# Performance work log

Hardware: AMD Instinct MI355X
Metric: run time of the kernel (lower is better)

## Reference

```python
import jax, jax.numpy as jnp
import numpy as np

B, S, H, E, K = 8, 4096, 1024, 256, 64
NEG = -1e30  # finite stand-in for -inf to keep grads NaN-free


def setup_inputs() -> dict:
    key = jax.random.key(0)
    ks = jax.random.split(key, 8)
    Hq = H // 4
    sc = 0.02
    return {
        "hidden_states": jax.random.normal(ks[0], (B, S, H), dtype=jnp.float32),
        "attention_mask": jnp.ones((B, S), dtype=jnp.int32),
        "block_boundaries": jnp.sort(jax.random.randint(ks[1], (B, K), 0, S), axis=-1),
        "tok_w1": jax.random.normal(ks[2], (H, Hq), dtype=jnp.float32) * sc,
        "tok_b1": jnp.zeros((Hq,), dtype=jnp.float32),
        "tok_w2": jax.random.normal(ks[3], (Hq, 1), dtype=jnp.float32) * sc,
        "tok_b2": jnp.zeros((1,), dtype=jnp.float32),
        "blk_w1": jax.random.normal(ks[4], (H, Hq), dtype=jnp.float32) * sc,
        "blk_b1": jnp.zeros((Hq,), dtype=jnp.float32),
        "blk_w2": jax.random.normal(ks[5], (Hq, 1), dtype=jnp.float32) * sc,
        "blk_b2": jnp.zeros((1,), dtype=jnp.float32),
        "out_w": jax.random.normal(ks[6], (H, E), dtype=jnp.float32) * sc,
        "out_b": jnp.zeros((E,), dtype=jnp.float32),
    }


def _attn_scores(x, w1, b1, w2, b2):
    # Linear -> Tanh -> Linear(.,1), squeeze last dim
    return (jnp.tanh(x @ w1 + b1) @ w2 + b2)[..., 0]


def reference(hidden_states, attention_mask, block_boundaries,
              tok_w1, tok_b1, tok_w2, tok_b2,
              blk_w1, blk_b1, blk_w2, blk_b2,
              out_w, out_b):
    Bz, Sz, Hz = hidden_states.shape
    Kz = block_boundaries.shape[1]
    pos = jnp.arange(Sz)
    # token -> block id: last boundary <= pos (tokens before first boundary get -1)
    block_id = jax.vmap(lambda bnd: jnp.searchsorted(bnd, pos, side='right') - 1)(block_boundaries)  # [B,S]
    member = block_id[:, :, None] == jnp.arange(Kz)[None, None, :]      # [B,S,K]
    valid = (attention_mask == 1) & (block_id >= 0)                     # [B,S]
    m_full = member & valid[:, :, None]                                 # [B,S,K]

    # stage 1: per-block masked softmax over tokens
    tok_scores = _attn_scores(hidden_states, tok_w1, tok_b1, tok_w2, tok_b2)  # [B,S]
    s = jnp.where(m_full, tok_scores[:, :, None], NEG)
    mx = jnp.max(s, axis=1, keepdims=True)                              # [B,1,K]
    e = jnp.where(m_full, jnp.exp(tok_scores[:, :, None] - mx), 0.0)
    denom = jnp.sum(e, axis=1, keepdims=True)                           # [B,1,K]
    w = jnp.where(denom > 0, e / jnp.maximum(denom, 1e-30), 0.0)
    block_embed = jnp.einsum('bsk,bsd->bkd', w, hidden_states)          # [B,K,H]
    block_valid = denom[:, 0, :] > 0                                    # [B,K] (empty blocks dropped)

    # stage 2: softmax over (non-empty) blocks
    blk_scores = _attn_scores(block_embed, blk_w1, blk_b1, blk_w2, blk_b2)    # [B,K]
    blk_scores = jnp.where(block_valid, blk_scores, NEG)
    bw = jax.nn.softmax(blk_scores, axis=-1)
    func = jnp.einsum('bk,bkd->bd', bw, block_embed)                    # [B,H]

    out = func @ out_w + out_b                                          # [B,E]
    return out / jnp.maximum(jnp.linalg.norm(out, axis=-1, keepdims=True), 1e-12)
```

## Files before the change

kernel.cpp:

```cpp
#include <hip/hip_runtime.h>
#include <math.h>
#include <limits.h>

#define BB 8
#define SS 4096
#define HH 1024
#define EE 256
#define KK 64
#define HQ 256
#define NEGF -1e30f

typedef short bf16x8 __attribute__((ext_vector_type(8)));
typedef float f32x4  __attribute__((ext_vector_type(4)));

__device__ inline short f2bf(float x) {
    unsigned u = __float_as_uint(x);
    unsigned r = (u + 0x7fffu + ((u >> 16) & 1u)) >> 16;
    return (short)r;
}

__device__ inline unsigned pk2bf(float lo, float hi) {
    unsigned a = __float_as_uint(lo) + 0x8000u;
    unsigned b = __float_as_uint(hi) + 0x8000u;
    return (a >> 16) | (b & 0xffff0000u);
}

__global__ __launch_bounds__(256) void convert_both_kernel(
    const float* __restrict__ tok_w1, const float* __restrict__ blk_w1,
    short* __restrict__ w1s_tok, short* __restrict__ w1s_blk)
{
    const int kb = blockIdx.x & 31, which = blockIdx.x >> 5;
    const float* src = which ? blk_w1 : tok_w1;
    short* dst = which ? w1s_blk : w1s_tok;
    const int n = threadIdx.x;
    for (int kk = 0; kk < 32; kk++)
        dst[kb * 8192 + n * 32 + kk] = f2bf(src[(kb * 32 + kk) * HQ + n]);
}

__global__ __launch_bounds__(256, 4) void mfma_score4_kernel(
    const float* __restrict__ X, const short* __restrict__ w1s,
    const float* __restrict__ b1, const float* __restrict__ w2,
    const float* __restrict__ b2, float* __restrict__ out)
{
    __shared__ __attribute__((aligned(16))) short As[2][4][1024];
    __shared__ float part[4][32];

    const int t = threadIdx.x;
    const int wv = t >> 6, lane = t & 63, lo = lane & 15, q = lane >> 4;
    const long row0 = (long)blockIdx.x * 32;

    f32x4 acc[2][4];
#pragma unroll
    for (int i = 0; i < 2; i++)
#pragma unroll
        for (int j = 0; j < 4; j++) acc[i][j] = (f32x4){0.f, 0.f, 0.f, 0.f};

    const int c = t >> 1, half = t & 1;
    const int srow = ((c >> 6) << 4) + (c & 15);
    const int skofs = ((c >> 4) & 3) * 8 + half * 4;
    const float* xs = X + (row0 + srow) * HH + skofs;
    const int dofs = c * 8 + half * 4;
    const short* wp = w1s + (wv * 64 + lo) * 32 + q * 8;

    float4 sv[4];
    bf16x8 bC[4], bN[4];

#pragma unroll
    for (int j = 0; j < 4; j++) sv[j] = *(const float4*)(xs + j * 32);
#pragma unroll
    for (int j = 0; j < 4; j++) {
        unsigned u0 = pk2bf(sv[j].x, sv[j].y), u1 = pk2bf(sv[j].z, sv[j].w);
        unsigned* d = (unsigned*)&As[0][j][dofs];
        d[0] = u0; d[1] = u1;
    }
#pragma unroll
    for (int j = 0; j < 4; j++) sv[j] = *(const float4*)(xs + (4 + j) * 32);
#pragma unroll
    for (int ct = 0; ct < 4; ct++) bC[ct] = *(const bf16x8*)(wp + ct * 512);
    asm volatile("s_waitcnt lgkmcnt(0)" ::: "memory");
    __builtin_amdgcn_sched_barrier(0);
    __builtin_amdgcn_s_barrier();
    __builtin_amdgcn_sched_barrier(0);

#define KSTEP(J, BUSE, BPRE, KBN)                                              \
    {                                                                          \
        _Pragma("unroll")                                                      \
        for (int ct = 0; ct < 4; ct++)                                         \
            BPRE[ct] = *(const bf16x8*)(wp + (KBN) * 8192 + ct * 512);         \
        bf16x8 af0 = *(const bf16x8*)&As[cur][J][(q * 16 + lo) * 8];           \
        bf16x8 af1 = *(const bf16x8*)&As[cur][J][(64 + q * 16 + lo) * 8];      \
        _Pragma("unroll")                                                      \
        for (int ct = 0; ct < 4; ct++) {                                       \
            acc[0][ct] = __builtin_amdgcn_mfma_f32_16x16x32_bf16(              \
                af0, BUSE[ct], acc[0][ct], 0, 0, 0);                           \
            acc[1][ct] = __builtin_amdgcn_mfma_f32_16x16x32_bf16(              \
                af1, BUSE[ct], acc[1][ct], 0, 0, 0);                           \
        }                                                                      \
    }

    for (int ci = 0; ci < 8; ci++) {
        const int cur = ci & 1;
        const int kb0 = ci * 4;
        KSTEP(0, bC, bN, kb0 + 1)
        KSTEP(1, bN, bC, kb0 + 2)
        KSTEP(2, bC, bN, kb0 + 3)
        const int kbn3 = (kb0 + 4 < 32) ? kb0 + 4 : 31;
        KSTEP(3, bN, bC, kbn3)
        if (ci < 7) {
#pragma unroll
            for (int j = 0; j < 4; j++) {
                unsigned u0 = pk2bf(sv[j].x, sv[j].y), u1 = pk2bf(sv[j].z, sv[j].w);
                unsigned* d = (unsigned*)&As[cur ^ 1][j][dofs];
                d[0] = u0; d[1] = u1;
            }
            const int cn = (ci + 2 < 8) ? ci + 2 : 7;
#pragma unroll
            for (int j = 0; j < 4; j++)
                sv[j] = *(const float4*)(xs + (cn * 4 + j) * 32);
        }
        asm volatile("s_waitcnt lgkmcnt(0)" ::: "memory");
        __builtin_amdgcn_sched_barrier(0);
        __builtin_amdgcn_s_barrier();
        __builtin_amdgcn_sched_barrier(0);
    }
#undef KSTEP

    float rowpart[2][4];
#pragma unroll
    for (int rt = 0; rt < 2; rt++)
#pragma unroll
        for (int r = 0; r < 4; r++) rowpart[rt][r] = 0.f;
#pragma unroll
    for (int ct = 0; ct < 4; ct++) {
        const int cc = wv * 64 + ct * 16 + lo;
        const float b1c = b1[cc], w2c = w2[cc];
#pragma unroll
        for (int rt = 0; rt < 2; rt++)
#pragma unroll
            for (int r = 0; r < 4; r++)
                rowpart[rt][r] += tanhf(acc[rt][ct][r] + b1c) * w2c;
    }
#pragma unroll
    for (int rt = 0; rt < 2; rt++)
#pragma unroll
        for (int r = 0; r < 4; r++) {
            float v = rowpart[rt][r];
            v += __shfl_down(v, 8, 64);
            v += __shfl_down(v, 4, 64);
            v += __shfl_down(v, 2, 64);
            v += __shfl_down(v, 1, 64);
            rowpart[rt][r] = v;
        }
    if (lo == 0)
#pragma unroll
        for (int rt = 0; rt < 2; rt++)
#pragma unroll
            for (int r = 0; r < 4; r++)
                part[wv][rt * 16 + q * 4 + r] = rowpart[rt][r];
    __syncthreads();
    if (t < 32)
        out[row0 + t] = part[0][t] + part[1][t] + part[2][t] + part[3][t] + b2[0];
}

__global__ __launch_bounds__(256) void block_stats_kernel(
    const float* __restrict__ scores, const int* __restrict__ mask,
    const int* __restrict__ bnd, float* __restrict__ bden,
    float* __restrict__ wtok, float* __restrict__ embed)
{
    const int b = blockIdx.x >> 6, k = blockIdx.x & 63;
    const int start = bnd[b * KK + k];
    const int end = (k == KK - 1) ? SS : bnd[b * KK + k + 1];
    const int tid = threadIdx.x;
    __shared__ float r[4];
    __shared__ float mshared, dshared;

    *((float4*)(embed + (long)blockIdx.x * HH) + tid) = (float4){0.f, 0.f, 0.f, 0.f};
    if (k == 0)
        for (int s = tid; s < start; s += 256) wtok[b * SS + s] = 0.f;

    float m = NEGF;
    for (int s = start + tid; s < end; s += 256)
        if (mask[b * SS + s] == 1) m = fmaxf(m, scores[b * SS + s]);
    for (int off = 32; off > 0; off >>= 1) m = fmaxf(m, __shfl_down(m, off, 64));
    if ((tid & 63) == 0) r[tid >> 6] = m;
    __syncthreads();
    if (tid == 0) mshared = fmaxf(fmaxf(r[0], r[1]), fmaxf(r[2], r[3]));
    __syncthreads();
    m = mshared;

    float d = 0.f;
    for (int s = start + tid; s < end; s += 256)
        if (mask[b * SS + s] == 1) d += expf(scores[b * SS + s] - m);
    for (int off = 32; off > 0; off >>= 1) d += __shfl_down(d, off, 64);
    __syncthreads();
    if ((tid & 63) == 0) r[tid >> 6] = d;
    __syncthreads();
    if (tid == 0) {
        float den = r[0] + r[1] + r[2] + r[3];
        bden[blockIdx.x] = den;
        dshared = (den > 0.f) ? 1.f / fmaxf(den, 1e-30f) : 0.f;
    }
    __syncthreads();
    const float inv = dshared;
    for (int s = start + tid; s < end; s += 256)
        wtok[b * SS + s] = (mask[b * SS + s] == 1) ? expf(scores[b * SS + s] - m) * inv : 0.f;
}

#define TCH 16
__global__ __launch_bounds__(256) void block_embed4_kernel(
    const float* __restrict__ hidden, const float* __restrict__ wtok,
    const int* __restrict__ bnd, float* __restrict__ embed)
{
    const int b = blockIdx.x >> 8;
    const int ch = blockIdx.x & 255;
    const int t = threadIdx.x;
    __shared__ int bsh[KK];
    __shared__ float wsh[TCH];
    const int s0 = ch * TCH, s1 = s0 + TCH;
    if (t < KK) bsh[t] = bnd[b * KK + t];
    if (t >= 64 && t < 64 + TCH) wsh[t - 64] = wtok[b * SS + s0 + (t - 64)];
    __syncthreads();

    int cur = -1;
#pragma unroll
    for (int i = 0; i < KK; i++) cur = (bsh[i] <= s0) ? i : cur;
    const int nxt = (cur + 1 < KK) ? bsh[cur + 1] : INT_MAX;

    const float* hr0 = hidden + ((long)b * SS + s0) * HH + t;
    float a0 = 0.f, a1 = 0.f, a2 = 0.f, a3 = 0.f;

    if (nxt >= s1 && cur >= 0) {
#pragma unroll
        for (int i = 0; i < TCH; i++) {
            const float w = wsh[i];
            const float* hr = hr0 + (long)i * HH;
            a0 = fmaf(w, hr[0], a0);
            a1 = fmaf(w, hr[256], a1);
            a2 = fmaf(w, hr[512], a2);
            a3 = fmaf(w, hr[768], a3);
        }
        float* e = embed + ((long)b * KK + cur) * HH;
        atomicAdd(e + t, a0); atomicAdd(e + t + 256, a1);
        atomicAdd(e + t + 512, a2); atomicAdd(e + t + 768, a3);
        return;
    }

    bool any = false;
    for (int s = s0; s < s1; s++) {
        while (cur + 1 < KK && bsh[cur + 1] <= s) {
            if (any) {
                float* e = embed + ((long)b * KK + cur) * HH;
                atomicAdd(e + t, a0); atomicAdd(e + t + 256, a1);
                atomicAdd(e + t + 512, a2); atomicAdd(e + t + 768, a3);
                a0 = a1 = a2 = a3 = 0.f; any = false;
            }
            cur++;
        }
        if (cur < 0) continue;
        const float w = wsh[s - s0];
        const float* hr = hr0 + (long)(s - s0) * HH;
        a0 = fmaf(w, hr[0], a0);
        a1 = fmaf(w, hr[256], a1);
        a2 = fmaf(w, hr[512], a2);
        a3 = fmaf(w, hr[768], a3);
        any = true;
    }
    if (any) {
        float* e = embed + ((long)b * KK + cur) * HH;
        atomicAdd(e + t, a0); atomicAdd(e + t + 256, a1);
        atomicAdd(e + t + 512, a2); atomicAdd(e + t + 768, a3);
    }
}

__global__ __launch_bounds__(256) void finalize_ab_kernel(
    const float* __restrict__ embed, const float* __restrict__ bscores,
    const float* __restrict__ bden, const float* __restrict__ out_w,
    float* __restrict__ osum)
{
    const int b = blockIdx.x >> 3, hc = blockIdx.x & 7;
    const int t = threadIdx.x;
    __shared__ float bw[KK];
    __shared__ float fpart[2][128];
    __shared__ float fsh[128];

    if (t < KK) {
        float s = (bden[b * KK + t] > 0.f) ? bscores[b * KK + t] : NEGF;
        float m = s;
        for (int off = 32; off > 0; off >>= 1) m = fmaxf(m, __shfl_xor(m, off, 64));
        float e = expf(s - m);
        float d = e;
        for (int off = 32; off > 0; off >>= 1) d += __shfl_xor(d, off, 64);
        bw[t] = e / d;
    }
    __syncthreads();

    {
        const int hh = t & 127, kh = t >> 7;
        const float* ep = embed + ((long)b * KK + kh * 32) * HH + hc * 128 + hh;
        float f = 0.f;
#pragma unroll 8
        for (int k2 = 0; k2 < 32; k2++)
            f = fmaf(bw[kh * 32 + k2], ep[(long)k2 * HH], f);
        fpart[kh][hh] = f;
    }
    __syncthreads();
    if (t < 128) fsh[t] = fpart[0][t] + fpart[1][t];
    __syncthreads();

    float acc = 0.f;
    const float* wpp = out_w + (long)(hc * 128) * EE + t;
#pragma unroll 8
    for (int h = 0; h < 128; h++)
        acc = fmaf(fsh[h], wpp[(long)h * EE], acc);
    osum[(long)(b * 8 + hc) * EE + t] = acc;
}

__global__ __launch_bounds__(256) void finalize_c_kernel(
    const float* __restrict__ osum, const float* __restrict__ out_b,
    float* __restrict__ outp)
{
    const int b = blockIdx.x, t = threadIdx.x;
    __shared__ float r4[4];
    float o = out_b[t];
#pragma unroll
    for (int hc = 0; hc < 8; hc++)
        o += osum[(long)(b * 8 + hc) * EE + t];
    float sq = o * o;
    for (int off = 32; off > 0; off >>= 1) sq += __shfl_down(sq, off, 64);
    if ((t & 63) == 0) r4[t >> 6] = sq;
    __syncthreads();
    const float nrm = sqrtf(r4[0] + r4[1] + r4[2] + r4[3]);
    outp[b * EE + t] = o / fmaxf(nrm, 1e-12f);
}

extern "C" void kernel_launch(void* const* d_in, const int* in_sizes, int n_in,
                              void* d_out, int out_size, void* d_ws, size_t ws_size,
                              hipStream_t stream) {
    const float* hidden  = (const float*)d_in[0];
    const int*   mask    = (const int*)  d_in[1];
    const int*   bnd     = (const int*)  d_in[2];
    const float* tok_w1  = (const float*)d_in[3];
    const float* tok_b1  = (const float*)d_in[4];
    const float* tok_w2  = (const float*)d_in[5];
    const float* tok_b2  = (const float*)d_in[6];
    const float* blk_w1  = (const float*)d_in[7];
    const float* blk_b1  = (const float*)d_in[8];
    const float* blk_w2  = (const float*)d_in[9];
    const float* blk_b2  = (const float*)d_in[10];
    const float* out_w   = (const float*)d_in[11];
    const float* out_b   = (const float*)d_in[12];

    float* ws      = (float*)d_ws;
    float* wtok    = ws;
    float* embed   = ws + 32768;
    float* scores  = ws + 557056;
    float* bden    = ws + 589824;
    float* bscores = ws + 590336;
    float* osum    = ws + 590848;
    short* w1s_tok = (short*)(ws + 607232);
    short* w1s_blk = w1s_tok + 262144;

    convert_both_kernel<<<64, 256, 0, stream>>>(tok_w1, blk_w1, w1s_tok, w1s_blk);
    mfma_score4_kernel<<<BB * SS / 32, 256, 0, stream>>>(
        hidden, w1s_tok, tok_b1, tok_w2, tok_b2, scores);
    block_stats_kernel<<<BB * KK, 256, 0, stream>>>(
        scores, mask, bnd, bden, wtok, embed);
    block_embed4_kernel<<<BB * SS / TCH, 256, 0, stream>>>(hidden, wtok, bnd, embed);
    mfma_score4_kernel<<<BB * KK / 32, 256, 0, stream>>>(
        embed, w1s_blk, blk_b1, blk_w2, blk_b2, bscores);
    finalize_ab_kernel<<<BB * 8, 256, 0, stream>>>(
        embed, bscores, bden, out_w, osum);
    finalize_c_kernel<<<BB, 256, 0, stream>>>(osum, out_b, (float*)d_out);
}
```

Measured before the change: 297.1 us.

## Enlarge score-GEMM row tile to 64 and deepen weight-fragment prefetch

The MFMA score kernel now processes 64 rows per workgroup instead of 32, so each weight fragment read from global memory feeds four row tiles instead of two. The staging layout changes to one 16-byte LDS store per thread per k-slice, and weight fragments are kept in registers four k-blocks ahead instead of one. This reduces global weight traffic per row and hides more load latency, at the cost of more accumulator and B registers (occupancy hint lowered to 2) and half as many workgroups. The small block-score launch drops to 8 workgroups.

```diff
diff --git a/kernel.cpp b/kernel.cpp
--- a/kernel.cpp
+++ b/kernel.cpp
@@ -37,97 +37,105 @@
         dst[kb * 8192 + n * 32 + kk] = f2bf(src[(kb * 32 + kk) * HQ + n]);
 }
 
-__global__ __launch_bounds__(256, 4) void mfma_score4_kernel(
+__global__ __launch_bounds__(256, 2) void mfma_score64_kernel(
     const float* __restrict__ X, const short* __restrict__ w1s,
     const float* __restrict__ b1, const float* __restrict__ w2,
     const float* __restrict__ b2, float* __restrict__ out)
 {
-    __shared__ __attribute__((aligned(16))) short As[2][4][1024];
-    __shared__ float part[4][32];
+    __shared__ __attribute__((aligned(16))) short As[2][4][2048];
+    __shared__ float part[4][64];
 
     const int t = threadIdx.x;
     const int wv = t >> 6, lane = t & 63, lo = lane & 15, q = lane >> 4;
-    const long row0 = (long)blockIdx.x * 32;
-
-    f32x4 acc[2][4];
-#pragma unroll
-    for (int i = 0; i < 2; i++)
+    const long row0 = (long)blockIdx.x * 64;
+
+    f32x4 acc[4][4];
+#pragma unroll
+    for (int i = 0; i < 4; i++)
 #pragma unroll
         for (int j = 0; j < 4; j++) acc[i][j] = (f32x4){0.f, 0.f, 0.f, 0.f};
 
-    const int c = t >> 1, half = t & 1;
-    const int srow = ((c >> 6) << 4) + (c & 15);
-    const int skofs = ((c >> 4) & 3) * 8 + half * 4;
-    const float* xs = X + (row0 + srow) * HH + skofs;
-    const int dofs = c * 8 + half * 4;
+    const int rt_s = t >> 6, q_s = (t >> 4) & 3, lo_s = t & 15;
+    const float* xs = X + (row0 + rt_s * 16 + lo_s) * HH + q_s * 8;
     const short* wp = w1s + (wv * 64 + lo) * 32 + q * 8;
 
-    float4 sv[4];
-    bf16x8 bC[4], bN[4];
-
-#pragma unroll
-    for (int j = 0; j < 4; j++) sv[j] = *(const float4*)(xs + j * 32);
-#pragma unroll
-    for (int j = 0; j < 4; j++) {
-        unsigned u0 = pk2bf(sv[j].x, sv[j].y), u1 = pk2bf(sv[j].z, sv[j].w);
-        unsigned* d = (unsigned*)&As[0][j][dofs];
-        d[0] = u0; d[1] = u1;
-    }
-#pragma unroll
-    for (int j = 0; j < 4; j++) sv[j] = *(const float4*)(xs + (4 + j) * 32);
-#pragma unroll
-    for (int ct = 0; ct < 4; ct++) bC[ct] = *(const bf16x8*)(wp + ct * 512);
+    float4 sv[4][2];
+    bf16x8 bR[4][4];
+
+#pragma unroll
+    for (int m = 0; m < 4; m++) {
+        sv[m][0] = *(const float4*)(xs + m * 32);
+        sv[m][1] = *(const float4*)(xs + m * 32 + 4);
+    }
+#pragma unroll
+    for (int m = 0; m < 4; m++) {
+        uint4 u;
+        u.x = pk2bf(sv[m][0].x, sv[m][0].y);
+        u.y = pk2bf(sv[m][0].z, sv[m][0].w);
+        u.z = pk2bf(sv[m][1].x, sv[m][1].y);
+        u.w = pk2bf(sv[m][1].z, sv[m][1].w);
+        *(uint4*)&As[0][m][t * 8] = u;
+    }
+#pragma unroll
+    for (int m = 0; m < 4; m++) {
+        sv[m][0] = *(const float4*)(xs + 128 + m * 32);
+        sv[m][1] = *(const float4*)(xs + 128 + m * 32 + 4);
+    }
+#pragma unroll
+    for (int kk = 0; kk < 4; kk++)
+#pragma unroll
+        for (int ct = 0; ct < 4; ct++)
+            bR[kk][ct] = *(const bf16x8*)(wp + kk * 8192 + ct * 512);
     asm volatile("s_waitcnt lgkmcnt(0)" ::: "memory");
     __builtin_amdgcn_sched_barrier(0);
     __builtin_amdgcn_s_barrier();
     __builtin_amdgcn_sched_barrier(0);
 
-#define KSTEP(J, BUSE, BPRE, KBN)                                              \
-    {                                                                          \
-        _Pragma("unroll")                                                      \
-        for (int ct = 0; ct < 4; ct++)                                         \
-            BPRE[ct] = *(const bf16x8*)(wp + (KBN) * 8192 + ct * 512);         \
-        bf16x8 af0 = *(const bf16x8*)&As[cur][J][(q * 16 + lo) * 8];           \
-        bf16x8 af1 = *(const bf16x8*)&As[cur][J][(64 + q * 16 + lo) * 8];      \
-        _Pragma("unroll")                                                      \
-        for (int ct = 0; ct < 4; ct++) {                                       \
-            acc[0][ct] = __builtin_amdgcn_mfma_f32_16x16x32_bf16(              \
-                af0, BUSE[ct], acc[0][ct], 0, 0, 0);                           \
-            acc[1][ct] = __builtin_amdgcn_mfma_f32_16x16x32_bf16(              \
-                af1, BUSE[ct], acc[1][ct], 0, 0, 0);                           \
-        }                                                                      \
-    }
-
     for (int ci = 0; ci < 8; ci++) {
         const int cur = ci & 1;
-        const int kb0 = ci * 4;
-        KSTEP(0, bC, bN, kb0 + 1)
-        KSTEP(1, bN, bC, kb0 + 2)
-        KSTEP(2, bC, bN, kb0 + 3)
-        const int kbn3 = (kb0 + 4 < 32) ? kb0 + 4 : 31;
-        KSTEP(3, bN, bC, kbn3)
+#pragma unroll
+        for (int j = 0; j < 4; j++) {
+            bf16x8 af[4];
+#pragma unroll
+            for (int rt = 0; rt < 4; rt++)
+                af[rt] = *(const bf16x8*)&As[cur][j][(rt * 64 + q * 16 + lo) * 8];
+#pragma unroll
+            for (int rt = 0; rt < 4; rt++)
+#pragma unroll
+                for (int ct = 0; ct < 4; ct++)
+                    acc[rt][ct] = __builtin_amdgcn_mfma_f32_16x16x32_bf16(
+                        af[rt], bR[j][ct], acc[rt][ct], 0, 0, 0);
+            const int kn = (ci * 4 + j + 4 < 32) ? ci * 4 + j + 4 : 31;
+#pragma unroll
+            for (int ct = 0; ct < 4; ct++)
+                bR[j][ct] = *(const bf16x8*)(wp + kn * 8192 + ct * 512);
+        }
         if (ci < 7) {
 #pragma unroll
-            for (int j = 0; j < 4; j++) {
-                unsigned u0 = pk2bf(sv[j].x, sv[j].y), u1 = pk2bf(sv[j].z, sv[j].w);
-                unsigned* d = (unsigned*)&As[cur ^ 1][j][dofs];
-                d[0] = u0; d[1] = u1;
+            for (int m = 0; m < 4; m++) {
+                uint4 u;
+                u.x = pk2bf(sv[m][0].x, sv[m][0].y);
+                u.y = pk2bf(sv[m][0].z, sv[m][0].w);
+                u.z = pk2bf(sv[m][1].x, sv[m][1].y);
+                u.w = pk2bf(sv[m][1].z, sv[m][1].w);
+                *(uint4*)&As[cur ^ 1][m][t * 8] = u;
             }
             const int cn = (ci + 2 < 8) ? ci + 2 : 7;
 #pragma unroll
-            for (int j = 0; j < 4; j++)
-                sv[j] = *(const float4*)(xs + (cn * 4 + j) * 32);
+            for (int m = 0; m < 4; m++) {
+                sv[m][0] = *(const float4*)(xs + cn * 128 + m * 32);
+                sv[m][1] = *(const float4*)(xs + cn * 128 + m * 32 + 4);
+            }
         }
         asm volatile("s_waitcnt lgkmcnt(0)" ::: "memory");
         __builtin_amdgcn_sched_barrier(0);
         __builtin_amdgcn_s_barrier();
         __builtin_amdgcn_sched_barrier(0);
     }
-#undef KSTEP
-
-    float rowpart[2][4];
-#pragma unroll
-    for (int rt = 0; rt < 2; rt++)
+
+    float rowpart[4][4];
+#pragma unroll
+    for (int rt = 0; rt < 4; rt++)
 #pragma unroll
         for (int r = 0; r < 4; r++) rowpart[rt][r] = 0.f;
 #pragma unroll
@@ -135,13 +143,13 @@
         const int cc = wv * 64 + ct * 16 + lo;
         const float b1c = b1[cc], w2c = w2[cc];
 #pragma unroll
-        for (int rt = 0; rt < 2; rt++)
+        for (int rt = 0; rt < 4; rt++)
 #pragma unroll
             for (int r = 0; r < 4; r++)
                 rowpart[rt][r] += tanhf(acc[rt][ct][r] + b1c) * w2c;
     }
 #pragma unroll
-    for (int rt = 0; rt < 2; rt++)
+    for (int rt = 0; rt < 4; rt++)
 #pragma unroll
         for (int r = 0; r < 4; r++) {
             float v = rowpart[rt][r];
@@ -153,12 +161,12 @@
         }
     if (lo == 0)
 #pragma unroll
-        for (int rt = 0; rt < 2; rt++)
+        for (int rt = 0; rt < 4; rt++)
 #pragma unroll
             for (int r = 0; r < 4; r++)
                 part[wv][rt * 16 + q * 4 + r] = rowpart[rt][r];
     __syncthreads();
-    if (t < 32)
+    if (t < 64)
         out[row0 + t] = part[0][t] + part[1][t] + part[2][t] + part[3][t] + b2[0];
 }
 
@@ -361,12 +369,12 @@
     short* w1s_blk = w1s_tok + 262144;
 
     convert_both_kernel<<<64, 256, 0, stream>>>(tok_w1, blk_w1, w1s_tok, w1s_blk);
-    mfma_score4_kernel<<<BB * SS / 32, 256, 0, stream>>>(
+    mfma_score64_kernel<<<BB * SS / 64, 256, 0, stream>>>(
         hidden, w1s_tok, tok_b1, tok_w2, tok_b2, scores);
     block_stats_kernel<<<BB * KK, 256, 0, stream>>>(
         scores, mask, bnd, bden, wtok, embed);
     block_embed4_kernel<<<BB * SS / TCH, 256, 0, stream>>>(hidden, wtok, bnd, embed);
-    mfma_score4_kernel<<<BB * KK / 32, 256, 0, stream>>>(
+    mfma_score64_kernel<<<BB * KK / 64, 256, 0, stream>>>(
         embed, w1s_blk, blk_b1, blk_w2, blk_b2, bscores);
     finalize_ab_kernel<<<BB * 8, 256, 0, stream>>>(
         embed, bscores, bden, out_w, osum);
```

New measurement: 298.1 us. Within noise of the previous version (+0.3%).
